# Kernel tuning notes

Measured on AMD Instinct MI355X. Metric: run time of the kernel, lower is better.

The kernel has to match this reference:

```python
import jax, jax.numpy as jnp
import numpy as np
from jax import lax

T_LOW, T_HIGH = 100.0, 200.0   # init kwargs of Canny
TG22 = 0.4142135623730951      # tan(22.5 deg), cv2's direction quantization constant
MAX_ITERS = 512                # safety cap on hysteresis fixed-point loop


def _shift(a, dy, dx):
    # neighbor value n[y, x] = a[y + dy, x + dx], zero outside
    H, W = a.shape
    p = jnp.pad(a, 1)
    return p[1 + dy:1 + dy + H, 1 + dx:1 + dx + W]


def _canny(x):
    B, C, H, W = x.shape
    # toRGB: ((x+1)/2*255).to(uint8)  (truncation; values are non-negative)
    img = jnp.clip(jnp.floor((x + 1.0) * 0.5 * 255.0), 0.0, 255.0)
    # original reshapes batch into one tall strip (B*H, W, C) before cv2.Canny
    img = img.transpose(0, 2, 3, 1).reshape(B * H, W, C)
    HH = B * H
    p = jnp.pad(img, ((1, 1), (1, 1), (0, 0)), mode='edge')  # replicate border like cv2

    def s(dy, dx):
        return p[1 + dy:1 + dy + HH, 1 + dx:1 + dx + W, :]

    # 3x3 Sobel per channel
    gx = (s(-1, 1) + 2.0 * s(0, 1) + s(1, 1)) - (s(-1, -1) + 2.0 * s(0, -1) + s(1, -1))
    gy = (s(1, -1) + 2.0 * s(1, 0) + s(1, 1)) - (s(-1, -1) + 2.0 * s(-1, 0) + s(-1, 1))
    mag_c = jnp.abs(gx) + jnp.abs(gy)  # L1 magnitude (cv2 default L2gradient=False)
    # multi-channel: take channel with max magnitude per pixel (cv2 behavior)
    idx = jnp.argmax(mag_c, axis=-1, keepdims=True)
    gx = jnp.take_along_axis(gx, idx, -1)[..., 0]
    gy = jnp.take_along_axis(gy, idx, -1)[..., 0]
    mag = jnp.take_along_axis(mag_c, idx, -1)[..., 0]

    # non-maximum suppression with 4 quantized directions
    ax_, ay_ = jnp.abs(gx), jnp.abs(gy)
    is_h = ay_ < TG22 * ax_          # gradient ~horizontal -> compare left/right
    is_v = ay_ * TG22 > ax_          # gradient ~vertical -> compare up/down
    same = (gx * gy) >= 0.0          # diagonal orientation by sign agreement
    n1 = jnp.where(is_h, _shift(mag, 0, -1),
         jnp.where(is_v, _shift(mag, -1, 0),
         jnp.where(same, _shift(mag, -1, -1), _shift(mag, -1, 1))))
    n2 = jnp.where(is_h, _shift(mag, 0, 1),
         jnp.where(is_v, _shift(mag, 1, 0),
         jnp.where(same, _shift(mag, 1, 1), _shift(mag, 1, -1))))
    keep = (mag > n1) & (mag >= n2)

    strong = keep & (mag > T_HIGH)
    weak = keep & (mag > T_LOW)

    # hysteresis: propagate strong labels through 8-connected weak pixels to fixed point
    def dilate(m):
        mf = m.astype(jnp.float32)
        return lax.reduce_window(mf, 0.0, lax.add, (3, 3), (1, 1), 'SAME') > 0.0

    def body(st):
        s0, _, it = st
        grown = (dilate(s0) & weak) | s0
        return grown, jnp.any(grown != s0), it + 1

    def cond(st):
        return st[1] & (st[2] < MAX_ITERS)

    strong, _, _ = lax.while_loop(cond, body, (strong, jnp.array(True), jnp.array(0)))

    edges = strong.reshape(B, H, W).astype(jnp.float32)        # {0,1} == cv2 {0,255}/255
    edges = jnp.broadcast_to(edges[:, None, :, :], (B, 3, H, W))
    return (edges - 0.5) / 0.5                                 # T.Normalize(0.5, 0.5)


def setup_inputs() -> dict:
    key = jax.random.key(0)
    x = jax.random.uniform(key, (16, 3, 512, 512), jnp.float32, -1.0, 1.0)
    return {"x": x}


def reference(x):
    return _canny(x)
```

## Files before the change

kernel.cpp:

```cpp
#include <hip/hip_runtime.h>
#include <stdint.h>

#define HH 8192
#define WW 512
#define WPR 8
#define TG22F 0.4142135623730951f
#define NROUND 8
#define NBLK 32


__device__ __forceinline__ float to_img(float v) {
    float t = floorf((v + 1.0f) * 0.5f * 255.0f);
    return fminf(fmaxf(t, 0.0f), 255.0f);
}

__device__ __forceinline__ int bsel(uint64_t w0, uint64_t w1, int idx) {
    return (idx < 8) ? (int)((w0 >> (idx * 8)) & 255)
                     : (int)((w1 >> ((idx - 8) * 8)) & 255);
}

__device__ __forceinline__ uint64_t runfill(uint64_t s, uint64_t w) {
    uint64_t sw = s & w;
    uint64_t up = ((sw + w) ^ w) & w;
    uint64_t rs = __brevll(sw);
    uint64_t rw = __brevll(w);
    uint64_t dn = __brevll(((rs + rw) ^ rw) & rw);
    return up | dn | sw;
}

__device__ __forceinline__ uint64_t shfl_up64(uint64_t v, int d) {
    int lo = __shfl_up((int)(uint32_t)v, d, 64);
    int hi = __shfl_up((int)(uint32_t)(v >> 32), d, 64);
    return ((uint64_t)(uint32_t)hi << 32) | (uint32_t)lo;
}
__device__ __forceinline__ uint64_t shfl_dn64(uint64_t v, int d) {
    int lo = __shfl_down((int)(uint32_t)v, d, 64);
    int hi = __shfl_down((int)(uint32_t)(v >> 32), d, 64);
    return ((uint64_t)(uint32_t)hi << 32) | (uint32_t)lo;
}

__device__ __forceinline__ uint64_t cload64(const unsigned long long* p) {
    return __hip_atomic_load((const unsigned long long*)p, __ATOMIC_RELAXED,
                             __HIP_MEMORY_SCOPE_AGENT);
}
__device__ __forceinline__ void cstore64(unsigned long long* p, uint64_t v) {
    __hip_atomic_store(p, (unsigned long long)v, __ATOMIC_RELAXED,
                       __HIP_MEMORY_SCOPE_AGENT);
}

__global__ void k_sobel(const float* __restrict__ in, uint16_t* __restrict__ packed) {
    __shared__ uint8_t simg[3 * 34 * 72];
    const int tid = threadIdx.x;
    const int row0 = (blockIdx.x >> 3) << 5;
    const int col0 = (blockIdx.x & 7) << 6;

    for (int i = tid; i < 1632; i += 256) {
        int c = i / 544;
        int rem = i - c * 544;
        int hr = rem >> 4;
        int q = rem & 15;
        int gy = row0 + hr - 1;
        gy = gy < 0 ? 0 : (gy >= HH ? HH - 1 : gy);
        int b = gy >> 9, h = gy & 511;
        const float4 v = *(const float4*)&in[((((b * 3 + c) << 9) + h) << 9) + col0 + (q << 2)];
        uint32_t pk = (uint32_t)(uint8_t)to_img(v.x)
                    | ((uint32_t)(uint8_t)to_img(v.y) << 8)
                    | ((uint32_t)(uint8_t)to_img(v.z) << 16)
                    | ((uint32_t)(uint8_t)to_img(v.w) << 24);
        *(uint32_t*)&simg[(c * 34 + hr) * 72 + 4 + (q << 2)] = pk;
    }
    for (int i = tid; i < 204; i += 256) {
        int c = i / 68;
        int rem = i - c * 68;
        int hr = rem >> 1;
        int side = rem & 1;
        int gy = row0 + hr - 1;
        gy = gy < 0 ? 0 : (gy >= HH ? HH - 1 : gy);
        int gc = side ? col0 + 64 : col0 - 1;
        gc = gc < 0 ? 0 : (gc >= WW ? WW - 1 : gc);
        int b = gy >> 9, h = gy & 511;
        float v = to_img(in[((((b * 3 + c) << 9) + h) << 9) + gc]);
        simg[(c * 34 + hr) * 72 + (side ? 68 : 3)] = (uint8_t)v;
    }
    __syncthreads();

    const int r = tid >> 3;
    const int c8 = (tid & 7) << 3;

    int bestMag[8], bgx[8], bgy[8];
    #pragma unroll
    for (int j = 0; j < 8; ++j) { bestMag[j] = -1; bgx[j] = 0; bgy[j] = 0; }

    #pragma unroll
    for (int c = 0; c < 3; ++c) {
        const uint8_t* base = &simg[(c * 34 + r) * 72 + c8];
        uint64_t w00 = *(const uint64_t*)(base);
        uint64_t w01 = *(const uint64_t*)(base + 8);
        uint64_t w10 = *(const uint64_t*)(base + 72);
        uint64_t w11 = *(const uint64_t*)(base + 80);
        uint64_t w20 = *(const uint64_t*)(base + 144);
        uint64_t w21 = *(const uint64_t*)(base + 152);
        int vs[10], t0[10], t2[10];
        #pragma unroll
        for (int i = 0; i < 10; ++i) {
            int a0 = bsel(w00, w01, 3 + i);
            int a1 = bsel(w10, w11, 3 + i);
            int a2 = bsel(w20, w21, 3 + i);
            vs[i] = a0 + 2 * a1 + a2;
            t0[i] = a0; t2[i] = a2;
        }
        #pragma unroll
        for (int j = 0; j < 8; ++j) {
            int gx = vs[j + 2] - vs[j];
            int gy = (t2[j] + 2 * t2[j + 1] + t2[j + 2]) - (t0[j] + 2 * t0[j + 1] + t0[j + 2]);
            int mg = abs(gx) + abs(gy);
            if (mg > bestMag[j]) { bestMag[j] = mg; bgx[j] = gx; bgy[j] = gy; }
        }
    }

    uint32_t res[4];
    #pragma unroll
    for (int jj = 0; jj < 4; ++jj) {
        uint32_t pair = 0;
        #pragma unroll
        for (int s = 0; s < 2; ++s) {
            int j = jj * 2 + s;
            float axf = (float)abs(bgx[j]);
            float ayf = (float)abs(bgy[j]);
            int dir;
            if (ayf < TG22F * axf)      dir = 0;
            else if (ayf * TG22F > axf) dir = 1;
            else                        dir = (bgx[j] * bgy[j] >= 0) ? 2 : 3;
            uint32_t val = (uint32_t)(bestMag[j] | (dir << 12));
            pair |= val << (s * 16);
        }
        res[jj] = pair;
    }
    int y = row0 + r;
    *(uint4*)&packed[y * WW + col0 + c8] = *(uint4*)res;
}

__global__ void k_nms(const uint16_t* __restrict__ packed,
                      unsigned long long* __restrict__ strongB,
                      unsigned long long* __restrict__ weakB,
                      int* __restrict__ flags) {
    if (blockIdx.x == 0 && threadIdx.x < 16) flags[threadIdx.x] = 0;
    int y = blockIdx.x >> 1;
    int x = ((blockIdx.x & 1) << 8) + threadIdx.x;
    uint16_t own = packed[y * WW + x];
    int mag = own & 0xFFF;
    int dir = own >> 12;
    int d1y = (dir == 0) ? 0 : -1;
    int d1x = (dir == 0) ? -1 : (dir == 1) ? 0 : (dir == 2) ? -1 : 1;
    int n1y = y + d1y, n1x = x + d1x;
    int n2y = y - d1y, n2x = x - d1x;
    int n1 = (n1y >= 0 && n1y < HH && n1x >= 0 && n1x < WW) ? (packed[n1y * WW + n1x] & 0xFFF) : 0;
    int n2 = (n2y >= 0 && n2y < HH && n2x >= 0 && n2x < WW) ? (packed[n2y * WW + n2x] & 0xFFF) : 0;
    bool keep = (mag > n1) && (mag >= n2);
    bool strong = keep && (mag > 200);
    bool weak   = keep && (mag > 100);
    unsigned long long sb = __ballot(strong ? 1 : 0);
    unsigned long long wb = __ballot(weak ? 1 : 0);
    if ((threadIdx.x & 63) == 0) {
        int word = y * WPR + (x >> 6);
        strongB[word] = sb;
        weakB[word]   = wb;
    }
}

__global__ void __launch_bounds__(256) k_hyst(
        const unsigned long long* __restrict__ weakB,
        unsigned long long* __restrict__ buf,
        int* __restrict__ flags)
{
    const int lane = threadIdx.x & 63;
    const int wave = (blockIdx.x << 2) + (threadIdx.x >> 6);
    const int base = ((wave << 6) + lane) * WPR;

    uint64_t own[8], wk[8];
    #pragma unroll
    for (int k = 0; k < 8; ++k) { wk[k] = weakB[base + k]; own[k] = buf[base + k]; }

    uint64_t hspu[8], hspd[8];
    #pragma unroll
    for (int k = 0; k < 8; ++k) { hspu[k] = 0; hspd[k] = 0; }

    auto load_halo = [&]() {
        uint64_t h[8];
        if (lane == 0 && wave > 0) {
            #pragma unroll
            for (int k = 0; k < 8; ++k) h[k] = cload64(&buf[base - WPR + k]);
            #pragma unroll
            for (int k = 0; k < 8; ++k) {
                uint64_t a = h[k] | (h[k] << 1) | (h[k] >> 1);
                if (k > 0) a |= h[k - 1] >> 63;
                if (k < 7) a |= h[k + 1] << 63;
                hspu[k] = a;
            }
        }
        if (lane == 63 && wave < 127) {
            #pragma unroll
            for (int k = 0; k < 8; ++k) h[k] = cload64(&buf[base + WPR + k]);
            #pragma unroll
            for (int k = 0; k < 8; ++k) {
                uint64_t a = h[k] | (h[k] << 1) | (h[k] >> 1);
                if (k > 0) a |= h[k - 1] >> 63;
                if (k < 7) a |= h[k + 1] << 63;
                hspd[k] = a;
            }
        }
    };
    load_halo();

    bool grewAny = false;
    for (int r = 0; r < NROUND; ++r) {
        bool grew = false;
        for (;;) {
            uint64_t sp[8];
            #pragma unroll
            for (int k = 0; k < 8; ++k) {
                uint64_t h = own[k] | (own[k] << 1) | (own[k] >> 1);
                if (k > 0) h |= own[k - 1] >> 63;
                if (k < 7) h |= own[k + 1] << 63;
                sp[k] = h;
            }
            uint64_t su[8], sd[8];
            #pragma unroll
            for (int k = 0; k < 8; ++k) {
                su[k] = shfl_up64(sp[k], 1);
                sd[k] = shfl_dn64(sp[k], 1);
            }
            if (lane == 0) {
                #pragma unroll
                for (int k = 0; k < 8; ++k) su[k] = hspu[k];
            }
            if (lane == 63) {
                #pragma unroll
                for (int k = 0; k < 8; ++k) sd[k] = hspd[k];
            }
            uint32_t ch = 0;
            #pragma unroll
            for (int k = 0; k < 8; ++k) {
                uint64_t acc = sp[k] | su[k] | sd[k];
                uint64_t nv = runfill(own[k] | (acc & wk[k]), wk[k]);
                ch |= (uint32_t)(nv != own[k]);
                own[k] = nv;
            }
            if (ch) grew = true;
            if (__ballot(ch ? 1 : 0) == 0ull) break;
        }
        grewAny |= grew;

        if (grew && lane == 0)
            __hip_atomic_store(&flags[r], 1, __ATOMIC_RELAXED, __HIP_MEMORY_SCOPE_AGENT);
        if (lane == 0 || lane == 63) {
            #pragma unroll
            for (int k = 0; k < 8; ++k) cstore64(&buf[base + k], own[k]);
        }
        __syncthreads();
        if (threadIdx.x == 0) {
            __hip_atomic_fetch_add(&flags[8 + r], 1, __ATOMIC_RELAXED, __HIP_MEMORY_SCOPE_AGENT);
            while (__hip_atomic_load(&flags[8 + r], __ATOMIC_RELAXED, __HIP_MEMORY_SCOPE_AGENT) < NBLK)
                __builtin_amdgcn_s_sleep(2);
        }
        __syncthreads();

        if (__hip_atomic_load(&flags[r], __ATOMIC_RELAXED, __HIP_MEMORY_SCOPE_AGENT) == 0)
            break;
        if (r + 1 < NROUND) load_halo();
    }

    if (__ballot(grewAny ? 1 : 0) != 0ull) {
        #pragma unroll
        for (int k = 0; k < 8; ++k) buf[base + k] = own[k];
    }
}

__global__ void k_out(const unsigned long long* __restrict__ result, float* __restrict__ out) {
    int t = blockIdx.x * blockDim.x + threadIdx.x;
    int b = t >> 16;
    int r = t & 65535;
    int h = r >> 7;
    int w = (r & 127) << 2;
    int y = (b << 9) + h;
    unsigned long long word = result[y * WPR + (w >> 6)];
    int sh = w & 63;
    float4 v;
    v.x = ((word >> (sh + 0)) & 1ull) ? 1.0f : -1.0f;
    v.y = ((word >> (sh + 1)) & 1ull) ? 1.0f : -1.0f;
    v.z = ((word >> (sh + 2)) & 1ull) ? 1.0f : -1.0f;
    v.w = ((word >> (sh + 3)) & 1ull) ? 1.0f : -1.0f;
    int base = (b * 3) << 18;
    int off = (h << 9) + w;
    *(float4*)&out[base + off] = v;
    *(float4*)&out[base + 262144 + off] = v;
    *(float4*)&out[base + 524288 + off] = v;
}

extern "C" void kernel_launch(void* const* d_in, const int* in_sizes, int n_in,
                              void* d_out, int out_size, void* d_ws, size_t ws_size,
                              hipStream_t stream) {
    const float* x = (const float*)d_in[0];
    float* out = (float*)d_out;
    char* ws = (char*)d_ws;

    uint16_t* packed          = (uint16_t*)(ws);
    unsigned long long* buf   = (unsigned long long*)(ws + 8388608);
    unsigned long long* weakB = (unsigned long long*)(ws + 8912896);
    int* flags                = (int*)(ws + 9437184);

    k_sobel<<<2048, 256, 0, stream>>>(x, packed);
    k_nms<<<HH * 2, 256, 0, stream>>>(packed, buf, weakB, flags);
    k_hyst<<<NBLK, 256, 0, stream>>>(weakB, buf, flags);
    k_out<<<4096, 256, 0, stream>>>(buf, out);
}
```

Before: 131.2 us.

## Fuse Sobel with NMS and fold output expansion into hysteresis kernel

Sobel and non-maximum suppression are combined into one kernel. It loads a 2-pixel halo and recomputes border magnitudes in shared memory, so the packed magnitude/direction buffer round trip and one launch go away. The separate output kernel is removed, and the hysteresis kernel writes the three-channel float output directly from its register bitmasks. The trade-off is that the large output write now runs from only 32 blocks, with each lane writing a different row, which cuts write parallelism and coalescing.

Measured after the change: 167.8 us. +27.8%, slower.

```diff
diff --git a/kernel.cpp b/kernel.cpp
--- a/kernel.cpp
+++ b/kernel.cpp
@@ -48,18 +48,27 @@
                        __HIP_MEMORY_SCOPE_AGENT);
 }
 
-__global__ void k_sobel(const float* __restrict__ in, uint16_t* __restrict__ packed) {
-    __shared__ uint8_t simg[3 * 34 * 72];
+__global__ void k_sobnms(const float* __restrict__ in,
+                         unsigned long long* __restrict__ strongB,
+                         unsigned long long* __restrict__ weakB,
+                         int* __restrict__ flags) {
+    __shared__ uint8_t  simg[3 * 36 * 80];
+    __shared__ uint16_t smag[34 * 68];
+    __shared__ uint8_t  sBm[32 * 8];
+    __shared__ uint8_t  wBm[32 * 8];
+
     const int tid = threadIdx.x;
     const int row0 = (blockIdx.x >> 3) << 5;
     const int col0 = (blockIdx.x & 7) << 6;
 
-    for (int i = tid; i < 1632; i += 256) {
-        int c = i / 544;
-        int rem = i - c * 544;
+    if (blockIdx.x == 0 && tid < 16) flags[tid] = 0;
+
+    for (int i = tid; i < 1728; i += 256) {
+        int c = i / 576;
+        int rem = i - c * 576;
         int hr = rem >> 4;
-        int q = rem & 15;
-        int gy = row0 + hr - 1;
+        int q  = rem & 15;
+        int gy = row0 + hr - 2;
         gy = gy < 0 ? 0 : (gy >= HH ? HH - 1 : gy);
         int b = gy >> 9, h = gy & 511;
         const float4 v = *(const float4*)&in[((((b * 3 + c) << 9) + h) << 9) + col0 + (q << 2)];
@@ -67,24 +76,25 @@
                     | ((uint32_t)(uint8_t)to_img(v.y) << 8)
                     | ((uint32_t)(uint8_t)to_img(v.z) << 16)
                     | ((uint32_t)(uint8_t)to_img(v.w) << 24);
-        *(uint32_t*)&simg[(c * 34 + hr) * 72 + 4 + (q << 2)] = pk;
-    }
-    for (int i = tid; i < 204; i += 256) {
-        int c = i / 68;
-        int rem = i - c * 68;
-        int hr = rem >> 1;
-        int side = rem & 1;
-        int gy = row0 + hr - 1;
+        *(uint32_t*)&simg[(c * 36 + hr) * 80 + 4 + (q << 2)] = pk;
+    }
+    for (int i = tid; i < 432; i += 256) {
+        int c = i / 144;
+        int rem = i - c * 144;
+        int hr = rem >> 2;
+        int e = rem & 3;
+        int gy = row0 + hr - 2;
         gy = gy < 0 ? 0 : (gy >= HH ? HH - 1 : gy);
-        int gc = side ? col0 + 64 : col0 - 1;
-        gc = gc < 0 ? 0 : (gc >= WW ? WW - 1 : gc);
+        int gx = col0 + ((e == 0) ? -2 : (e == 1) ? -1 : (e == 2) ? 64 : 65);
+        gx = gx < 0 ? 0 : (gx >= WW ? WW - 1 : gx);
         int b = gy >> 9, h = gy & 511;
-        float v = to_img(in[((((b * 3 + c) << 9) + h) << 9) + gc]);
-        simg[(c * 34 + hr) * 72 + (side ? 68 : 3)] = (uint8_t)v;
+        float v = to_img(in[((((b * 3 + c) << 9) + h) << 9) + gx]);
+        int off = (e == 0) ? 2 : (e == 1) ? 3 : (e == 2) ? 68 : 69;
+        simg[(c * 36 + hr) * 80 + off] = (uint8_t)v;
     }
     __syncthreads();
 
-    const int r = tid >> 3;
+    const int r  = tid >> 3;
     const int c8 = (tid & 7) << 3;
 
     int bestMag[8], bgx[8], bgy[8];
@@ -93,13 +103,13 @@
 
     #pragma unroll
     for (int c = 0; c < 3; ++c) {
-        const uint8_t* base = &simg[(c * 34 + r) * 72 + c8];
+        const uint8_t* base = &simg[(c * 36 + r + 1) * 80 + c8];
         uint64_t w00 = *(const uint64_t*)(base);
         uint64_t w01 = *(const uint64_t*)(base + 8);
-        uint64_t w10 = *(const uint64_t*)(base + 72);
-        uint64_t w11 = *(const uint64_t*)(base + 80);
-        uint64_t w20 = *(const uint64_t*)(base + 144);
-        uint64_t w21 = *(const uint64_t*)(base + 152);
+        uint64_t w10 = *(const uint64_t*)(base + 80);
+        uint64_t w11 = *(const uint64_t*)(base + 88);
+        uint64_t w20 = *(const uint64_t*)(base + 160);
+        uint64_t w21 = *(const uint64_t*)(base + 168);
         int vs[10], t0[10], t2[10];
         #pragma unroll
         for (int i = 0; i < 10; ++i) {
@@ -117,61 +127,73 @@
             if (mg > bestMag[j]) { bestMag[j] = mg; bgx[j] = gx; bgy[j] = gy; }
         }
     }
-
-    uint32_t res[4];
-    #pragma unroll
-    for (int jj = 0; jj < 4; ++jj) {
-        uint32_t pair = 0;
-        #pragma unroll
-        for (int s = 0; s < 2; ++s) {
-            int j = jj * 2 + s;
-            float axf = (float)abs(bgx[j]);
-            float ayf = (float)abs(bgy[j]);
-            int dir;
-            if (ayf < TG22F * axf)      dir = 0;
-            else if (ayf * TG22F > axf) dir = 1;
-            else                        dir = (bgx[j] * bgy[j] >= 0) ? 2 : 3;
-            uint32_t val = (uint32_t)(bestMag[j] | (dir << 12));
-            pair |= val << (s * 16);
-        }
-        res[jj] = pair;
-    }
-    int y = row0 + r;
-    *(uint4*)&packed[y * WW + col0 + c8] = *(uint4*)res;
-}
-
-__global__ void k_nms(const uint16_t* __restrict__ packed,
-                      unsigned long long* __restrict__ strongB,
-                      unsigned long long* __restrict__ weakB,
-                      int* __restrict__ flags) {
-    if (blockIdx.x == 0 && threadIdx.x < 16) flags[threadIdx.x] = 0;
-    int y = blockIdx.x >> 1;
-    int x = ((blockIdx.x & 1) << 8) + threadIdx.x;
-    uint16_t own = packed[y * WW + x];
-    int mag = own & 0xFFF;
-    int dir = own >> 12;
-    int d1y = (dir == 0) ? 0 : -1;
-    int d1x = (dir == 0) ? -1 : (dir == 1) ? 0 : (dir == 2) ? -1 : 1;
-    int n1y = y + d1y, n1x = x + d1x;
-    int n2y = y - d1y, n2x = x - d1x;
-    int n1 = (n1y >= 0 && n1y < HH && n1x >= 0 && n1x < WW) ? (packed[n1y * WW + n1x] & 0xFFF) : 0;
-    int n2 = (n2y >= 0 && n2y < HH && n2x >= 0 && n2x < WW) ? (packed[n2y * WW + n2x] & 0xFFF) : 0;
-    bool keep = (mag > n1) && (mag >= n2);
-    bool strong = keep && (mag > 200);
-    bool weak   = keep && (mag > 100);
-    unsigned long long sb = __ballot(strong ? 1 : 0);
-    unsigned long long wb = __ballot(weak ? 1 : 0);
-    if ((threadIdx.x & 63) == 0) {
-        int word = y * WPR + (x >> 6);
-        strongB[word] = sb;
-        weakB[word]   = wb;
+    #pragma unroll
+    for (int j = 0; j < 8; ++j)
+        smag[(r + 1) * 68 + (c8 + 1 + j)] = (uint16_t)bestMag[j];
+
+    if (tid < 196) {
+        int h, j;
+        if (tid < 66)       { h = 0;        j = tid; }
+        else if (tid < 132) { h = 33;       j = tid - 66; }
+        else if (tid < 164) { h = tid - 131; j = 0; }
+        else                { h = tid - 163; j = 65; }
+        int gy = row0 + h - 1, gx = col0 + j - 1;
+        int mg = 0;
+        if (gy >= 0 && gy < HH && gx >= 0 && gx < WW) {
+            #pragma unroll
+            for (int c = 0; c < 3; ++c) {
+                const uint8_t* p = &simg[(c * 36 + h) * 80 + (j + 2)];
+                int a00 = p[0],   a01 = p[1],   a02 = p[2];
+                int a10 = p[80],                a12 = p[82];
+                int a20 = p[160], a21 = p[161], a22 = p[162];
+                int gxx = (a02 + 2 * a12 + a22) - (a00 + 2 * a10 + a20);
+                int gyy = (a20 + 2 * a21 + a22) - (a00 + 2 * a01 + a02);
+                int m = abs(gxx) + abs(gyy);
+                if (m > mg) mg = m;
+            }
+        }
+        smag[h * 68 + j] = (uint16_t)mg;
+    }
+    __syncthreads();
+
+    uint32_t sbyte = 0, wbyte = 0;
+    #pragma unroll
+    for (int j = 0; j < 8; ++j) {
+        int mag = bestMag[j];
+        float axf = (float)abs(bgx[j]);
+        float ayf = (float)abs(bgy[j]);
+        int dir;
+        if (ayf < TG22F * axf)      dir = 0;
+        else if (ayf * TG22F > axf) dir = 1;
+        else                        dir = (bgx[j] * bgy[j] >= 0) ? 2 : 3;
+        int d1y = (dir == 0) ? 0 : -1;
+        int d1x = (dir == 0) ? -1 : (dir == 1) ? 0 : (dir == 2) ? -1 : 1;
+        int hh0 = r + 1, cc0 = c8 + 1 + j;
+        int n1 = smag[(hh0 + d1y) * 68 + (cc0 + d1x)];
+        int n2 = smag[(hh0 - d1y) * 68 + (cc0 - d1x)];
+        bool keep = (mag > n1) && (mag >= n2);
+        if (keep && mag > 200) sbyte |= 1u << j;
+        if (keep && mag > 100) wbyte |= 1u << j;
+    }
+    sBm[r * 8 + (tid & 7)] = (uint8_t)sbyte;
+    wBm[r * 8 + (tid & 7)] = (uint8_t)wbyte;
+    __syncthreads();
+
+    if (tid < 32) {
+        uint64_t wS = *(const uint64_t*)&sBm[tid * 8];
+        strongB[(row0 + tid) * WPR + (col0 >> 6)] = wS;
+    } else if (tid >= 64 && tid < 96) {
+        int t = tid - 64;
+        uint64_t wW = *(const uint64_t*)&wBm[t * 8];
+        weakB[(row0 + t) * WPR + (col0 >> 6)] = wW;
     }
 }
 
 __global__ void __launch_bounds__(256) k_hyst(
         const unsigned long long* __restrict__ weakB,
         unsigned long long* __restrict__ buf,
-        int* __restrict__ flags)
+        int* __restrict__ flags,
+        float* __restrict__ out)
 {
     const int lane = threadIdx.x & 63;
     const int wave = (blockIdx.x << 2) + (threadIdx.x >> 6);
@@ -212,7 +234,6 @@
     };
     load_halo();
 
-    bool grewAny = false;
     for (int r = 0; r < NROUND; ++r) {
         bool grew = false;
         for (;;) {
@@ -249,7 +270,6 @@
             if (ch) grew = true;
             if (__ballot(ch ? 1 : 0) == 0ull) break;
         }
-        grewAny |= grew;
 
         if (grew && lane == 0)
             __hip_atomic_store(&flags[r], 1, __ATOMIC_RELAXED, __HIP_MEMORY_SCOPE_AGENT);
@@ -270,31 +290,26 @@
         if (r + 1 < NROUND) load_halo();
     }
 
-    if (__ballot(grewAny ? 1 : 0) != 0ull) {
+    const int y = (wave << 6) + lane;
+    const int b = y >> 9, h = y & 511;
+    const int obase = ((b * 3) << 18) + (h << 9);
+    #pragma unroll
+    for (int k = 0; k < 8; ++k) {
+        uint64_t wv = own[k];
         #pragma unroll
-        for (int k = 0; k < 8; ++k) buf[base + k] = own[k];
-    }
-}
-
-__global__ void k_out(const unsigned long long* __restrict__ result, float* __restrict__ out) {
-    int t = blockIdx.x * blockDim.x + threadIdx.x;
-    int b = t >> 16;
-    int r = t & 65535;
-    int h = r >> 7;
-    int w = (r & 127) << 2;
-    int y = (b << 9) + h;
-    unsigned long long word = result[y * WPR + (w >> 6)];
-    int sh = w & 63;
-    float4 v;
-    v.x = ((word >> (sh + 0)) & 1ull) ? 1.0f : -1.0f;
-    v.y = ((word >> (sh + 1)) & 1ull) ? 1.0f : -1.0f;
-    v.z = ((word >> (sh + 2)) & 1ull) ? 1.0f : -1.0f;
-    v.w = ((word >> (sh + 3)) & 1ull) ? 1.0f : -1.0f;
-    int base = (b * 3) << 18;
-    int off = (h << 9) + w;
-    *(float4*)&out[base + off] = v;
-    *(float4*)&out[base + 262144 + off] = v;
-    *(float4*)&out[base + 524288 + off] = v;
+        for (int q = 0; q < 16; ++q) {
+            int x = (k << 6) + (q << 2);
+            int sh = q << 2;
+            float4 v;
+            v.x = ((wv >> (sh + 0)) & 1ull) ? 1.0f : -1.0f;
+            v.y = ((wv >> (sh + 1)) & 1ull) ? 1.0f : -1.0f;
+            v.z = ((wv >> (sh + 2)) & 1ull) ? 1.0f : -1.0f;
+            v.w = ((wv >> (sh + 3)) & 1ull) ? 1.0f : -1.0f;
+            *(float4*)&out[obase + x] = v;
+            *(float4*)&out[obase + (1 << 18) + x] = v;
+            *(float4*)&out[obase + (2 << 18) + x] = v;
+        }
+    }
 }
 
 extern "C" void kernel_launch(void* const* d_in, const int* in_sizes, int n_in,
@@ -304,13 +319,10 @@
     float* out = (float*)d_out;
     char* ws = (char*)d_ws;
 
-    uint16_t* packed          = (uint16_t*)(ws);
-    unsigned long long* buf   = (unsigned long long*)(ws + 8388608);
-    unsigned long long* weakB = (unsigned long long*)(ws + 8912896);
-    int* flags                = (int*)(ws + 9437184);
-
-    k_sobel<<<2048, 256, 0, stream>>>(x, packed);
-    k_nms<<<HH * 2, 256, 0, stream>>>(packed, buf, weakB, flags);
-    k_hyst<<<NBLK, 256, 0, stream>>>(weakB, buf, flags);
-    k_out<<<4096, 256, 0, stream>>>(buf, out);
-}
+    unsigned long long* buf   = (unsigned long long*)(ws);
+    unsigned long long* weakB = (unsigned long long*)(ws + 524288);
+    int* flags                = (int*)(ws + 1048576);
+
+    k_sobnms<<<2048, 256, 0, stream>>>(x, buf, weakB, flags);
+    k_hyst<<<NBLK, 256, 0, stream>>>(weakB, buf, flags, out);
+}
```
